# Kernel tuning notes

Measured on AMD Instinct MI355X. Metric: run time of the kernel, lower is better.

Reference implementation:

```python
import jax, jax.numpy as jnp
import numpy as np

N_NODES = 500_000
N_EDGES = 8_000_000
N_GRAPHS = 1000


def _mlp(x, w1, b1, w2, b2):
    # Linear -> SELU -> Linear (torch Sequential equivalent)
    return jax.nn.selu(x @ w1 + b1) @ w2 + b2


def setup_inputs() -> dict:
    key = jax.random.key(0)
    ks = jax.random.split(key, 25)
    p = lambda i, shape: jax.random.normal(ks[i], shape, jnp.float32) * 0.1
    return {
        "nodes": jax.random.normal(ks[0], (N_NODES, 1), jnp.float32),
        "edges": jax.random.normal(ks[1], (N_EDGES, 1), jnp.float32),
        "senders": jax.random.randint(ks[2], (N_EDGES,), 0, N_NODES),
        "receivers": jax.random.randint(ks[3], (N_EDGES,), 0, N_NODES),
        "graph_ids": jnp.sort(jax.random.randint(ks[4], (N_NODES,), 0, N_GRAPHS)),
        "num_graphs": N_GRAPHS,
        # permutate_nodes: 2 -> 10 -> 10
        "pn_w1": p(5, (2, 10)), "pn_b1": p(6, (10,)), "pn_w2": p(7, (10, 10)), "pn_b2": p(8, (10,)),
        # update_edges: 11 -> 5 -> 1
        "ue_w1": p(9, (11, 5)), "ue_b1": p(10, (5,)), "ue_w2": p(11, (5, 1)), "ue_b2": p(12, (1,)),
        # permutate_edges: 1 -> 5 -> 10
        "pe_w1": p(13, (1, 5)), "pe_b1": p(14, (5,)), "pe_w2": p(15, (5, 10)), "pe_b2": p(16, (10,)),
        # update_nodes: 11 -> 5 -> 1
        "un_w1": p(17, (11, 5)), "un_b1": p(18, (5,)), "un_w2": p(19, (5, 1)), "un_b2": p(20, (1,)),
        # predict: 11 -> 10 -> 10
        "pr_w1": p(21, (11, 10)), "pr_b1": p(22, (10,)), "pr_w2": p(23, (10, 10)), "pr_b2": p(24, (10,)),
    }


def reference(nodes, edges, pn_w1, pn_b1, pn_w2, pn_b2,
              ue_w1, ue_b1, ue_w2, ue_b2,
              pe_w1, pe_b1, pe_w2, pe_b2,
              un_w1, un_b1, un_w2, un_b2,
              pr_w1, pr_b1, pr_w2, pr_b2,
              senders, receivers, graph_ids, num_graphs):
    # gather node feats to edges: [recv || send] -> (E, 2)
    collected = jnp.concatenate([nodes[receivers], nodes[senders]], axis=-1)
    h1_nodes = _mlp(collected, pn_w1, pn_b1, pn_w2, pn_b2)  # (E, 10)
    h1_edges = edges  # (E, 1)
    for _ in range(3):
        h1_edges = _mlp(jnp.concatenate([h1_edges, h1_nodes], axis=-1),
                        ue_w1, ue_b1, ue_w2, ue_b2)  # (E, 1)
    # edges -> nodes aggregation (sum over receiver)
    edges_of_nodes = jax.ops.segment_sum(h1_edges, receivers, num_segments=nodes.shape[0])  # (N, 1)
    h2_edges = _mlp(edges_of_nodes, pe_w1, pe_b1, pe_w2, pe_b2)  # (N, 10)
    h2_nodes = nodes  # (N, 1)
    for _ in range(3):
        h2_nodes = _mlp(jnp.concatenate([h2_nodes, h2_edges], axis=-1),
                        un_w1, un_b1, un_w2, un_b2)  # (N, 1)
    # nodes -> globals aggregation (sum per graph)
    g = jax.ops.segment_sum(jnp.concatenate([h2_nodes, h2_edges], axis=-1),
                            graph_ids, num_segments=num_graphs)  # (G, 11)
    out = _mlp(g, pr_w1, pr_b1, pr_w2, pr_b2)  # (G, 10)
    return jax.nn.softmax(out, axis=-1)
```

## Files before the change

kernel.cpp:

```cpp
#include <hip/hip_runtime.h>
#include <hip/hip_fp16.h>
#include <math.h>

#define N_NODES_C  500000
#define N_EDGES_C  8000000
#define N_GRAPHS_C 1000
#define NGROUPS_C  (N_EDGES_C / 4)

#define BSHIFT  11
#define BWIDTH  2048
#define NBKT    245

#define PART_TPB 512
#define EPB     16384
#define GPB     (EPB / 4)
#define NPB     ((NGROUPS_C + GPB - 1) / GPB)
#define SROW    496
#define RITER   (GPB / PART_TPB)

#define GRAPH_ACC_OFF 0
#define PARTIALS_OFF  11008
#define FW_OFF        33024
#define STARTS_OFF    33280
#define PAIRS_OFF     (STARTS_OFF + 246 * SROW)
#define WS_WORDS_NEEDED (PAIRS_OFF + NPB * EPB)
#define ZERO_HEAD     33024
#define OLD_NODE_ACC_OFF 33536
#define OLD_ZERO_WORDS   (OLD_NODE_ACC_OFF + N_NODES_C)

#define LOG2E_F 1.4426950408889634f


__device__ __forceinline__ float selu2(float xl) {
    const float C1 = 0.7282901039f;
    const float C2 = 1.7580993408473766f;
    float e = __builtin_amdgcn_exp2f(xl);
    float neg = fmaf(C2, e, -C2);
    return xl > 0.0f ? C1 * xl : neg;
}

__device__ __forceinline__ float selu_f(float x) {
    const float scale = 1.0507009873554805f;
    const float sa    = 1.0507009873554805f * 1.6732632423543772f;
    float neg = sa * (__expf(x) - 1.0f);
    return x > 0.0f ? scale * x : neg;
}

__device__ __forceinline__ void atomAddF(float* p, float v) {
    __hip_atomic_fetch_add(p, v, __ATOMIC_RELAXED, __HIP_MEMORY_SCOPE_AGENT);
}

__device__ __forceinline__ void fuse_weights(
        int t,
        const float* __restrict__ pn_w1, const float* __restrict__ pn_b1,
        const float* __restrict__ pn_w2, const float* __restrict__ pn_b2,
        const float* __restrict__ ue_w1, const float* __restrict__ ue_b1,
        const float* __restrict__ ue_w2, const float* __restrict__ ue_b2,
        const float* __restrict__ pe_w1, const float* __restrict__ pe_b1,
        const float* __restrict__ pe_w2, const float* __restrict__ pe_b2,
        const float* __restrict__ un_w1, const float* __restrict__ un_b1,
        const float* __restrict__ un_w2, const float* __restrict__ un_b2,
        float* __restrict__ fw) {
    const float L = LOG2E_F;
    if (t < 20) fw[0 + t] = pn_w1[t] * L;
    if (t < 10) fw[20 + t] = pn_b1[t] * L;
    if (t < 50) {
        int j = t / 5, k = t % 5;
        float s = 0.0f;
        for (int m = 0; m < 10; ++m) s += pn_w2[j * 10 + m] * ue_w1[(1 + m) * 5 + k];
        fw[30 + t] = s * L;
    }
    if (t < 5) {
        float s = ue_b1[t];
        for (int m = 0; m < 10; ++m) s += pn_b2[m] * ue_w1[(1 + m) * 5 + t];
        fw[80 + t] = s * L;
    }
    if (t < 5)  fw[85 + t]  = ue_w1[t] * L;
    if (t < 5)  fw[90 + t]  = ue_w2[t];
    if (t == 0) fw[95]      = ue_b2[0];
    if (t < 5)  fw[96 + t]  = pe_w1[t] * L;
    if (t < 5)  fw[101 + t] = pe_b1[t] * L;
    if (t < 50) fw[106 + t] = pe_w2[t];
    if (t < 10) fw[156 + t] = pe_b2[t];
    if (t < 25) {
        int j = t / 5, k = t % 5;
        float s = 0.0f;
        for (int m = 0; m < 10; ++m) s += pe_w2[j * 10 + m] * un_w1[(1 + m) * 5 + k];
        fw[166 + t] = s * L;
    }
    if (t < 5) {
        float s = un_b1[t];
        for (int m = 0; m < 10; ++m) s += pe_b2[m] * un_w1[(1 + m) * 5 + t];
        fw[191 + t] = s * L;
    }
    if (t < 5)  fw[196 + t] = un_w1[t] * L;
    if (t < 5)  fw[201 + t] = un_w2[t];
    if (t == 0) fw[206]     = un_b2[0];
}

__global__ __launch_bounds__(256) void k_init(
        float* __restrict__ ws,
        const float* pn_w1, const float* pn_b1, const float* pn_w2, const float* pn_b2,
        const float* ue_w1, const float* ue_b1, const float* ue_w2, const float* ue_b2,
        const float* pe_w1, const float* pe_b1, const float* pe_w2, const float* pe_b2,
        const float* un_w1, const float* un_b1, const float* un_w2, const float* un_b2) {
    int i = blockIdx.x * 256 + threadIdx.x;
    if (i < ZERO_HEAD) ws[i] = 0.0f;
    if (blockIdx.x == 0)
        fuse_weights(threadIdx.x, pn_w1, pn_b1, pn_w2, pn_b2, ue_w1, ue_b1, ue_w2, ue_b2,
                     pe_w1, pe_b1, pe_w2, pe_b2, un_w1, un_b1, un_w2, un_b2, ws + FW_OFF);
}

__global__ void k_fuse(const float* pn_w1, const float* pn_b1, const float* pn_w2, const float* pn_b2,
                       const float* ue_w1, const float* ue_b1, const float* ue_w2, const float* ue_b2,
                       const float* pe_w1, const float* pe_b1, const float* pe_w2, const float* pe_b2,
                       const float* un_w1, const float* un_b1, const float* un_w2, const float* un_b2,
                       float* fw) {
    fuse_weights(threadIdx.x, pn_w1, pn_b1, pn_w2, pn_b2, ue_w1, ue_b1, ue_w2, ue_b2,
                 pe_w1, pe_b1, pe_w2, pe_b2, un_w1, un_b1, un_w2, un_b2, fw);
}

__global__ void k_final(const float* __restrict__ graph_acc,
                        const float* __restrict__ partials,
                        const float* __restrict__ pr_w1, const float* __restrict__ pr_b1,
                        const float* __restrict__ pr_w2, const float* __restrict__ pr_b2,
                        float* __restrict__ out) {
    int g = blockIdx.x * blockDim.x + threadIdx.x;
    if (g >= N_GRAPHS_C) return;
    float gv[11];
#pragma unroll
    for (int f = 0; f < 11; ++f)
        gv[f] = graph_acc[g * 11 + f] + partials[g * 11 + f] + partials[11000 + g * 11 + f];
    float h[10];
#pragma unroll
    for (int j = 0; j < 10; ++j) {
        float z = pr_b1[j];
#pragma unroll
        for (int f = 0; f < 11; ++f) z = fmaf(gv[f], pr_w1[f * 10 + j], z);
        h[j] = selu_f(z);
    }
    float o[10];
    float mx = -1e30f;
#pragma unroll
    for (int j = 0; j < 10; ++j) {
        float z = pr_b2[j];
#pragma unroll
        for (int m = 0; m < 10; ++m) z = fmaf(h[m], pr_w2[m * 10 + j], z);
        o[j] = z;
        mx = fmaxf(mx, z);
    }
    float sum = 0.0f;
#pragma unroll
    for (int j = 0; j < 10; ++j) { o[j] = __expf(o[j] - mx); sum += o[j]; }
    float inv = 1.0f / sum;
#pragma unroll
    for (int j = 0; j < 10; ++j) out[g * 10 + j] = o[j] * inv;
}


__global__ __launch_bounds__(PART_TPB, 4) void k_part(
        const float* __restrict__ nodes, const float* __restrict__ edges,
        const int* __restrict__ senders, const int* __restrict__ receivers,
        const float* __restrict__ fw, int* __restrict__ starts_T,
        unsigned int* __restrict__ pairs) {
    __shared__ int hist[256];
    __shared__ int cursorS[256];
    __shared__ unsigned int staged[EPB];

    int tid = threadIdx.x;
    int p   = blockIdx.x;
    int gstart = p * GPB;
    int gnum   = NGROUPS_C - gstart;
    if (gnum > GPB) gnum = GPB;

    float w_pn1[20], b_pn1[10], W_eb[50], b_eb[5], w1r0[5], w2e[5];
#pragma unroll
    for (int j = 0; j < 20; ++j) w_pn1[j] = fw[j];
#pragma unroll
    for (int j = 0; j < 10; ++j) b_pn1[j] = fw[20 + j];
#pragma unroll
    for (int j = 0; j < 50; ++j) W_eb[j] = fw[30 + j];
#pragma unroll
    for (int j = 0; j < 5; ++j) b_eb[j] = fw[80 + j];
#pragma unroll
    for (int j = 0; j < 5; ++j) w1r0[j] = fw[85 + j];
#pragma unroll
    for (int j = 0; j < 5; ++j) w2e[j] = fw[90 + j];
    float b2e = fw[95];

    if (tid < 256) hist[tid] = 0;
    __syncthreads();

#pragma unroll 1
    for (int r = 0; r < RITER; ++r) {
        int idx = r * PART_TPB + tid;
        int gi  = gstart + (idx < gnum ? idx : 0);
        int4 rv = ((const int4*)receivers)[gi];
        if (idx < gnum) {
            atomicAdd(&hist[rv.x >> BSHIFT], 1);
            atomicAdd(&hist[rv.y >> BSHIFT], 1);
            atomicAdd(&hist[rv.z >> BSHIFT], 1);
            atomicAdd(&hist[rv.w >> BSHIFT], 1);
        }
    }
    __syncthreads();

    int orig = 0, val = 0;
    if (tid < 256) { orig = hist[tid]; val = orig; }
    for (int d = 1; d < 256; d <<= 1) {
        int add = 0;
        if (tid >= d && tid < 256) add = hist[tid - d];
        __syncthreads();
        if (tid >= d && tid < 256) { val += add; hist[tid] = val; }
        __syncthreads();
    }
    int excl = val - orig;
    if (tid < 256) cursorS[tid] = excl;
    if (tid < 246) starts_T[tid * SROW + p] = excl;
    __syncthreads();

    float4 e4A, e4B, e4N;
    int4   s4A, s4B, s4N, r4A, r4B, r4N;
    float  nsA0, nsA1, nsA2, nsA3, nrA0, nrA1, nrA2, nrA3;
    float  nsB0, nsB1, nsB2, nsB3, nrB0, nrB1, nrB2, nrB3;

    {
        int gi0 = gstart + (tid < gnum ? tid : 0);
        e4A = ((const float4*)edges)[gi0];
        s4A = ((const int4*)senders)[gi0];
        r4A = ((const int4*)receivers)[gi0];
        nsA0 = nodes[s4A.x]; nsA1 = nodes[s4A.y];
        nsA2 = nodes[s4A.z]; nsA3 = nodes[s4A.w];
        nrA0 = nodes[r4A.x]; nrA1 = nodes[r4A.y];
        nrA2 = nodes[r4A.z]; nrA3 = nodes[r4A.w];
        int idx1 = PART_TPB + tid;
        int gi1 = gstart + (idx1 < gnum ? idx1 : 0);
        e4B = ((const float4*)edges)[gi1];
        s4B = ((const int4*)senders)[gi1];
        r4B = ((const int4*)receivers)[gi1];
    }

#pragma unroll 1
    for (int r = 0; r < RITER; ++r) {
        {
            int idx2 = (r + 2) * PART_TPB + tid;
            int gi2  = gstart + (idx2 < gnum ? idx2 : 0);
            e4N = ((const float4*)edges)[gi2];
            s4N = ((const int4*)senders)[gi2];
            r4N = ((const int4*)receivers)[gi2];
        }
        nsB0 = nodes[s4B.x]; nsB1 = nodes[s4B.y];
        nsB2 = nodes[s4B.z]; nsB3 = nodes[s4B.w];
        nrB0 = nodes[r4B.x]; nrB1 = nodes[r4B.y];
        nrB2 = nodes[r4B.z]; nrB3 = nodes[r4B.w];

        float ev[4]  = {e4A.x, e4A.y, e4A.z, e4A.w};
        int   rv[4]  = {r4A.x, r4A.y, r4A.z, r4A.w};
        float nsv[4] = {nsA0, nsA1, nsA2, nsA3};
        float nrv[4] = {nrA0, nrA1, nrA2, nrA3};

        bool validr = (r * PART_TPB + tid) < gnum;
#pragma unroll
        for (int u = 0; u < 4; ++u) {
            float nr = nrv[u], ns = nsv[u];
            float bs[5];
#pragma unroll
            for (int k = 0; k < 5; ++k) bs[k] = b_eb[k];
#pragma unroll
            for (int j = 0; j < 10; ++j) {
                float zl = fmaf(nr, w_pn1[j], fmaf(ns, w_pn1[10 + j], b_pn1[j]));
                float sz = selu2(zl);
#pragma unroll
                for (int k = 0; k < 5; ++k) bs[k] = fmaf(sz, W_eb[j * 5 + k], bs[k]);
            }
            float e = ev[u];
#pragma unroll
            for (int it = 0; it < 3; ++it) {
                float acc2 = b2e;
#pragma unroll
                for (int k = 0; k < 5; ++k) {
                    float tt = selu2(fmaf(e, w1r0[k], bs[k]));
                    acc2 = fmaf(tt, w2e[k], acc2);
                }
                e = acc2;
            }
            if (validr) {
                int bkt  = rv[u] >> BSHIFT;
                int slot = atomicAdd(&cursorS[bkt], 1);
                unsigned int pk = ((unsigned int)(rv[u] & (BWIDTH - 1)) << 16)
                                | (unsigned int)__half_as_ushort(__float2half_rn(e));
                staged[slot] = pk;
            }
        }

        e4A = e4B; s4A = s4B; r4A = r4B;
        nsA0 = nsB0; nsA1 = nsB1; nsA2 = nsB2; nsA3 = nsB3;
        nrA0 = nrB0; nrA1 = nrB1; nrA2 = nrB2; nrA3 = nrB3;
        e4B = e4N; s4B = s4N; r4B = r4N;
    }
    __syncthreads();

    const uint4* staged4 = (const uint4*)staged;
    uint4* dst = (uint4*)(pairs + (size_t)p * EPB);
    for (int i = tid; i < gnum; i += PART_TPB) dst[i] = staged4[i];
}

__global__ __launch_bounds__(1024) void k_gather(
        const float* __restrict__ nodes, const int* __restrict__ graph_ids,
        const float* __restrict__ fw, const int* __restrict__ starts_T,
        const unsigned int* __restrict__ pairs, float* __restrict__ graph_acc,
        float* __restrict__ partials) {
    __shared__ float accf[BWIDTH];
    __shared__ int s0[SROW], s1[SROW];
    __shared__ float garr[32 * 11];
    int tid = threadIdx.x;
    int b   = blockIdx.x;

    accf[tid] = 0.0f; accf[1024 + tid] = 0.0f;
    if (tid < 352) garr[tid] = 0.0f;
    for (int i = tid; i < NPB; i += 1024) {
        s0[i] = starts_T[b * SROW + i];
        s1[i] = starts_T[(b + 1) * SROW + i];
    }
    __syncthreads();

    int g32 = tid >> 5, lane = tid & 31;
    for (int p = g32; p < NPB; p += 32) {
        int st = s0[p], en = s1[p];
        const unsigned int* seg = pairs + (size_t)p * EPB + st;
        int cnt = en - st;
        for (int i = lane; i < cnt; i += 32) {
            unsigned int pk = seg[i];
            atomicAdd(&accf[(pk >> 16) & (BWIDTH - 1)],
                      __half2float(__ushort_as_half((unsigned short)(pk & 0xffff))));
        }
    }
    __syncthreads();

    float w_pe1[5], b_pe1[5], pe_w2[50], pe_b2[10], W_nb[25], b_nb[5], w1r0n[5], w2n[5];
#pragma unroll
    for (int j = 0; j < 5; ++j) w_pe1[j] = fw[96 + j];
#pragma unroll
    for (int j = 0; j < 5; ++j) b_pe1[j] = fw[101 + j];
#pragma unroll
    for (int j = 0; j < 50; ++j) pe_w2[j] = fw[106 + j];
#pragma unroll
    for (int j = 0; j < 10; ++j) pe_b2[j] = fw[156 + j];
#pragma unroll
    for (int j = 0; j < 25; ++j) W_nb[j] = fw[166 + j];
#pragma unroll
    for (int j = 0; j < 5; ++j) b_nb[j] = fw[191 + j];
#pragma unroll
    for (int j = 0; j < 5; ++j) w1r0n[j] = fw[196 + j];
#pragma unroll
    for (int j = 0; j < 5; ++j) w2n[j] = fw[201 + j];
    float b2n = fw[206];

    int nodeBase = b << BSHIFT;
    int lastIdx  = nodeBase + BWIDTH;
    if (lastIdx > N_NODES_C) lastIdx = N_NODES_C;
    int gidBase = graph_ids[nodeBase];
    int gidEnd  = graph_ids[lastIdx - 1];

#pragma unroll
    for (int q = 0; q < 2; ++q) {
        int local = q * 1024 + tid;
        int i = nodeBase + local;
        bool valid = i < N_NODES_C;

        float s = accf[local];
        float t5[5];
#pragma unroll
        for (int k = 0; k < 5; ++k) t5[k] = selu2(fmaf(s, w_pe1[k], b_pe1[k]));
        float he[10];
#pragma unroll
        for (int m = 0; m < 10; ++m) {
            float a = pe_b2[m];
#pragma unroll
            for (int k = 0; k < 5; ++k) a = fmaf(t5[k], pe_w2[k * 10 + m], a);
            he[m] = a;
        }
        float bs[5];
#pragma unroll
        for (int k = 0; k < 5; ++k) {
            float a = b_nb[k];
#pragma unroll
            for (int t = 0; t < 5; ++t) a = fmaf(t5[t], W_nb[t * 5 + k], a);
            bs[k] = a;
        }
        float n = valid ? nodes[i] : 0.0f;
#pragma unroll
        for (int it = 0; it < 3; ++it) {
            float a = b2n;
#pragma unroll
            for (int k = 0; k < 5; ++k) {
                float tt = selu2(fmaf(n, w1r0n[k], bs[k]));
                a = fmaf(tt, w2n[k], a);
            }
            n = a;
        }

        int gid = valid ? graph_ids[i] : -1;
        if (!valid) {
            n = 0.0f;
#pragma unroll
            for (int m = 0; m < 10; ++m) he[m] = 0.0f;
        }

        int gid0 = __shfl(gid, 0, 64);
        bool allsame = __all(gid == gid0) && (gid0 >= 0);
        if (allsame) {
            float v = n;
#pragma unroll
            for (int off = 32; off > 0; off >>= 1) v += __shfl_down(v, off, 64);
            float vh[10];
#pragma unroll
            for (int m = 0; m < 10; ++m) {
                float ww = he[m];
#pragma unroll
                for (int off = 32; off > 0; off >>= 1) ww += __shfl_down(ww, off, 64);
                vh[m] = ww;
            }
            if ((tid & 63) == 0) {
                int off = gid0 - gidBase;
                if (off >= 0 && off < 32) {
                    atomicAdd(&garr[off * 11 + 0], v);
#pragma unroll
                    for (int m = 0; m < 10; ++m) atomicAdd(&garr[off * 11 + 1 + m], vh[m]);
                } else {
                    atomAddF(&graph_acc[gid0 * 11 + 0], v);
#pragma unroll
                    for (int m = 0; m < 10; ++m) atomAddF(&graph_acc[gid0 * 11 + 1 + m], vh[m]);
                }
            }
        } else if (valid) {
            int off = gid - gidBase;
            if (off >= 0 && off < 32) {
                atomicAdd(&garr[off * 11 + 0], n);
#pragma unroll
                for (int m = 0; m < 10; ++m) atomicAdd(&garr[off * 11 + 1 + m], he[m]);
            } else {
                atomAddF(&graph_acc[gid * 11 + 0], n);
#pragma unroll
                for (int m = 0; m < 10; ++m) atomAddF(&graph_acc[gid * 11 + 1 + m], he[m]);
            }
        }
    }
    __syncthreads();

    int ngl = gidEnd - gidBase + 1;
    if (ngl > 32) ngl = 32;
    int par = (b & 1) * 11000;
    for (int t = tid; t < ngl * 11; t += 1024) {
        int off = t / 11, f = t - off * 11;
        partials[par + (gidBase + off) * 11 + f] = garr[t];
    }
}


__global__ __launch_bounds__(256) void k_zero(float* __restrict__ ws, int len4) {
    int i = blockIdx.x * 256 + threadIdx.x;
    if (i < len4) ((float4*)ws)[i] = make_float4(0.f, 0.f, 0.f, 0.f);
}

__global__ __launch_bounds__(256) void k_edges(
        const float* __restrict__ nodes, const float* __restrict__ edges,
        const int* __restrict__ senders, const int* __restrict__ receivers,
        const float* __restrict__ fw, float* __restrict__ node_acc) {
    float w_pn1[20], b_pn1[10], W_eb[50], b_eb[5], w1r0[5], w2e[5];
#pragma unroll
    for (int j = 0; j < 20; ++j) w_pn1[j] = fw[j];
#pragma unroll
    for (int j = 0; j < 10; ++j) b_pn1[j] = fw[20 + j];
#pragma unroll
    for (int j = 0; j < 50; ++j) W_eb[j] = fw[30 + j];
#pragma unroll
    for (int j = 0; j < 5; ++j) b_eb[j] = fw[80 + j];
#pragma unroll
    for (int j = 0; j < 5; ++j) w1r0[j] = fw[85 + j];
#pragma unroll
    for (int j = 0; j < 5; ++j) w2e[j] = fw[90 + j];
    float b2e = fw[95];

    int g = blockIdx.x * 256 + threadIdx.x;
    if (g >= NGROUPS_C) return;

    float4 e4 = ((const float4*)edges)[g];
    int4  s4 = ((const int4*)senders)[g];
    int4  r4 = ((const int4*)receivers)[g];
    float ev[4] = {e4.x, e4.y, e4.z, e4.w};
    int   sv[4] = {s4.x, s4.y, s4.z, s4.w};
    int   rv[4] = {r4.x, r4.y, r4.z, r4.w};
    float nsv[4], nrv[4];
#pragma unroll
    for (int u = 0; u < 4; ++u) { nsv[u] = nodes[sv[u]]; nrv[u] = nodes[rv[u]]; }
#pragma unroll
    for (int u = 0; u < 4; ++u) {
        float nr = nrv[u], ns = nsv[u];
        float bs[5];
#pragma unroll
        for (int k = 0; k < 5; ++k) bs[k] = b_eb[k];
#pragma unroll
        for (int j = 0; j < 10; ++j) {
            float zl = fmaf(nr, w_pn1[j], fmaf(ns, w_pn1[10 + j], b_pn1[j]));
            float sz = selu2(zl);
#pragma unroll
            for (int k = 0; k < 5; ++k) bs[k] = fmaf(sz, W_eb[j * 5 + k], bs[k]);
        }
        float e = ev[u];
#pragma unroll
        for (int it = 0; it < 3; ++it) {
            float acc2 = b2e;
#pragma unroll
            for (int k = 0; k < 5; ++k) {
                float tt = selu2(fmaf(e, w1r0[k], bs[k]));
                acc2 = fmaf(tt, w2e[k], acc2);
            }
            e = acc2;
        }
        atomAddF(&node_acc[rv[u]], e);
    }
}

__global__ __launch_bounds__(256) void k_nodes(
        const float* __restrict__ nodes, const int* __restrict__ graph_ids,
        const float* __restrict__ fw, const float* __restrict__ node_acc,
        float* __restrict__ graph_acc) {
    float w_pe1[5], b_pe1[5], pe_w2[50], pe_b2[10], W_nb[25], b_nb[5], w1r0n[5], w2n[5];
#pragma unroll
    for (int j = 0; j < 5; ++j) w_pe1[j] = fw[96 + j];
#pragma unroll
    for (int j = 0; j < 5; ++j) b_pe1[j] = fw[101 + j];
#pragma unroll
    for (int j = 0; j < 50; ++j) pe_w2[j] = fw[106 + j];
#pragma unroll
    for (int j = 0; j < 10; ++j) pe_b2[j] = fw[156 + j];
#pragma unroll
    for (int j = 0; j < 25; ++j) W_nb[j] = fw[166 + j];
#pragma unroll
    for (int j = 0; j < 5; ++j) b_nb[j] = fw[191 + j];
#pragma unroll
    for (int j = 0; j < 5; ++j) w1r0n[j] = fw[196 + j];
#pragma unroll
    for (int j = 0; j < 5; ++j) w2n[j] = fw[201 + j];
    float b2n = fw[206];

    int i = blockIdx.x * 256 + threadIdx.x;
    bool valid = i < N_NODES_C;
    int ii = valid ? i : (N_NODES_C - 1);

    float s = node_acc[ii];
    float t5[5];
#pragma unroll
    for (int k = 0; k < 5; ++k) t5[k] = selu2(fmaf(s, w_pe1[k], b_pe1[k]));
    float he[10];
#pragma unroll
    for (int m = 0; m < 10; ++m) {
        float a = pe_b2[m];
#pragma unroll
        for (int k = 0; k < 5; ++k) a = fmaf(t5[k], pe_w2[k * 10 + m], a);
        he[m] = a;
    }
    float bs[5];
#pragma unroll
    for (int k = 0; k < 5; ++k) {
        float a = b_nb[k];
#pragma unroll
        for (int t = 0; t < 5; ++t) a = fmaf(t5[t], W_nb[t * 5 + k], a);
        bs[k] = a;
    }
    float n = nodes[ii];
#pragma unroll
    for (int it = 0; it < 3; ++it) {
        float a = b2n;
#pragma unroll
        for (int k = 0; k < 5; ++k) {
            float tt = selu2(fmaf(n, w1r0n[k], bs[k]));
            a = fmaf(tt, w2n[k], a);
        }
        n = a;
    }

    int gid = valid ? graph_ids[ii] : -1;
    if (!valid) {
        n = 0.0f;
#pragma unroll
        for (int m = 0; m < 10; ++m) he[m] = 0.0f;
    }

    int gid0 = __shfl(gid, 0, 64);
    bool allsame = __all(gid == gid0) && (gid0 >= 0);
    if (allsame) {
        float v = n;
#pragma unroll
        for (int off = 32; off > 0; off >>= 1) v += __shfl_down(v, off, 64);
        float vh[10];
#pragma unroll
        for (int m = 0; m < 10; ++m) {
            float ww = he[m];
#pragma unroll
            for (int off = 32; off > 0; off >>= 1) ww += __shfl_down(ww, off, 64);
            vh[m] = ww;
        }
        if ((threadIdx.x & 63) == 0) {
            atomAddF(&graph_acc[gid0 * 11 + 0], v);
#pragma unroll
            for (int m = 0; m < 10; ++m) atomAddF(&graph_acc[gid0 * 11 + 1 + m], vh[m]);
        }
    } else if (valid) {
        atomAddF(&graph_acc[gid * 11 + 0], n);
#pragma unroll
        for (int m = 0; m < 10; ++m) atomAddF(&graph_acc[gid * 11 + 1 + m], he[m]);
    }
}


extern "C" void kernel_launch(void* const* d_in, const int* in_sizes, int n_in,
                              void* d_out, int out_size, void* d_ws, size_t ws_size,
                              hipStream_t stream) {
    const float* nodes     = (const float*)d_in[0];
    const float* edges     = (const float*)d_in[1];
    const int*   senders   = (const int*)d_in[2];
    const int*   receivers = (const int*)d_in[3];
    const int*   graph_ids = (const int*)d_in[4];
    const float* pn_w1 = (const float*)d_in[6];
    const float* pn_b1 = (const float*)d_in[7];
    const float* pn_w2 = (const float*)d_in[8];
    const float* pn_b2 = (const float*)d_in[9];
    const float* ue_w1 = (const float*)d_in[10];
    const float* ue_b1 = (const float*)d_in[11];
    const float* ue_w2 = (const float*)d_in[12];
    const float* ue_b2 = (const float*)d_in[13];
    const float* pe_w1 = (const float*)d_in[14];
    const float* pe_b1 = (const float*)d_in[15];
    const float* pe_w2 = (const float*)d_in[16];
    const float* pe_b2 = (const float*)d_in[17];
    const float* un_w1 = (const float*)d_in[18];
    const float* un_b1 = (const float*)d_in[19];
    const float* un_w2 = (const float*)d_in[20];
    const float* un_b2 = (const float*)d_in[21];
    const float* pr_w1 = (const float*)d_in[22];
    const float* pr_b1 = (const float*)d_in[23];
    const float* pr_w2 = (const float*)d_in[24];
    const float* pr_b2 = (const float*)d_in[25];

    float* ws        = (float*)d_ws;
    float* graph_acc = ws + GRAPH_ACC_OFF;
    float* partials  = ws + PARTIALS_OFF;
    float* fw        = ws + FW_OFF;
    float* outp      = (float*)d_out;

    if (ws_size >= (size_t)WS_WORDS_NEEDED * 4) {
        int* starts_T        = (int*)ws + STARTS_OFF;
        unsigned int* pairs  = (unsigned int*)ws + PAIRS_OFF;

        hipLaunchKernelGGL(k_init, dim3((ZERO_HEAD + 255) / 256), dim3(256), 0, stream, ws,
                           pn_w1, pn_b1, pn_w2, pn_b2, ue_w1, ue_b1, ue_w2, ue_b2,
                           pe_w1, pe_b1, pe_w2, pe_b2, un_w1, un_b1, un_w2, un_b2);
        hipLaunchKernelGGL(k_part, dim3(NPB), dim3(PART_TPB), 0, stream,
                           nodes, edges, senders, receivers, fw, starts_T, pairs);
        hipLaunchKernelGGL(k_gather, dim3(NBKT), dim3(1024), 0, stream,
                           nodes, graph_ids, fw, starts_T, pairs, graph_acc, partials);
        hipLaunchKernelGGL(k_final, dim3((N_GRAPHS_C + 255) / 256), dim3(256), 0, stream,
                           graph_acc, partials, pr_w1, pr_b1, pr_w2, pr_b2, outp);
    } else {
        float* node_acc = ws + OLD_NODE_ACC_OFF;
        int len4 = OLD_ZERO_WORDS / 4;
        hipLaunchKernelGGL(k_zero, dim3((len4 + 255) / 256), dim3(256), 0, stream, ws, len4);
        hipLaunchKernelGGL(k_fuse, dim3(1), dim3(64), 0, stream,
                           pn_w1, pn_b1, pn_w2, pn_b2, ue_w1, ue_b1, ue_w2, ue_b2,
                           pe_w1, pe_b1, pe_w2, pe_b2, un_w1, un_b1, un_w2, un_b2, fw);
        hipLaunchKernelGGL(k_edges, dim3((NGROUPS_C + 255) / 256), dim3(256), 0, stream,
                           nodes, edges, senders, receivers, fw, node_acc);
        hipLaunchKernelGGL(k_nodes, dim3((N_NODES_C + 255) / 256), dim3(256), 0, stream,
                           nodes, graph_ids, fw, node_acc, graph_acc);
        hipLaunchKernelGGL(k_final, dim3((N_GRAPHS_C + 255) / 256), dim3(256), 0, stream,
                           graph_acc, partials, pr_w1, pr_b1, pr_w2, pr_b2, outp);
    }
}
```

Before: 318.9 us.

## Defer edge MLP to gather stage using 64-bit packed raw edge records

Measured after the change: 293.2 us. 1.09x faster.

```diff
diff --git a/kernel.cpp b/kernel.cpp
--- a/kernel.cpp
+++ b/kernel.cpp
@@ -18,13 +18,26 @@
 #define SROW    496
 #define RITER   (GPB / PART_TPB)
 
+#define P2_TPB  512
+#define EPB2    8192
+#define GPB2    (EPB2 / 4)
+#define NPB2    ((NGROUPS_C + GPB2 - 1) / GPB2)
+#define SROW2   992
+#define RITER2  (GPB2 / P2_TPB)
+
 #define GRAPH_ACC_OFF 0
 #define PARTIALS_OFF  11008
 #define FW_OFF        33024
+#define ZERO_HEAD     33024
+
 #define STARTS_OFF    33280
 #define PAIRS_OFF     (STARTS_OFF + 246 * SROW)
 #define WS_WORDS_NEEDED (PAIRS_OFF + NPB * EPB)
-#define ZERO_HEAD     33024
+
+#define STARTS2_OFF   33280
+#define PAIRS64_OFF   (STARTS2_OFF + 246 * SROW2)
+#define WS2_WORDS_NEEDED (PAIRS64_OFF + NPB2 * EPB2 * 2)
+
 #define OLD_NODE_ACC_OFF 33536
 #define OLD_ZERO_WORDS   (OLD_NODE_ACC_OFF + N_NODES_C)
 
@@ -155,6 +168,304 @@
     float inv = 1.0f / sum;
 #pragma unroll
     for (int j = 0; j < 10; ++j) out[g * 10 + j] = o[j] * inv;
+}
+
+
+__global__ __launch_bounds__(P2_TPB) void k_part2(
+        const float* __restrict__ edges,
+        const int* __restrict__ senders, const int* __restrict__ receivers,
+        int* __restrict__ starts_T, unsigned long long* __restrict__ pairs64) {
+    __shared__ int hist[256];
+    __shared__ int cursorS[256];
+    __shared__ alignas(16) unsigned long long staged[EPB2];
+
+    int tid = threadIdx.x;
+    int p   = blockIdx.x;
+    int gstart = p * GPB2;
+    int gnum   = NGROUPS_C - gstart;
+    if (gnum > GPB2) gnum = GPB2;
+
+    if (tid < 256) hist[tid] = 0;
+    __syncthreads();
+
+    int4 rv4[RITER2];
+#pragma unroll
+    for (int r = 0; r < RITER2; ++r) {
+        int idx = r * P2_TPB + tid;
+        int gi  = gstart + (idx < gnum ? idx : 0);
+        rv4[r] = ((const int4*)receivers)[gi];
+        if (idx < gnum) {
+            atomicAdd(&hist[rv4[r].x >> BSHIFT], 1);
+            atomicAdd(&hist[rv4[r].y >> BSHIFT], 1);
+            atomicAdd(&hist[rv4[r].z >> BSHIFT], 1);
+            atomicAdd(&hist[rv4[r].w >> BSHIFT], 1);
+        }
+    }
+    __syncthreads();
+
+    int orig = 0, val = 0;
+    if (tid < 256) { orig = hist[tid]; val = orig; }
+    for (int d = 1; d < 256; d <<= 1) {
+        int add = 0;
+        if (tid >= d && tid < 256) add = hist[tid - d];
+        __syncthreads();
+        if (tid >= d && tid < 256) { val += add; hist[tid] = val; }
+        __syncthreads();
+    }
+    int excl = val - orig;
+    if (tid < 256) cursorS[tid] = excl;
+    if (tid < 246) starts_T[tid * SROW2 + p] = excl;
+    __syncthreads();
+
+#pragma unroll
+    for (int r = 0; r < RITER2; ++r) {
+        int idx = r * P2_TPB + tid;
+        int gi  = gstart + (idx < gnum ? idx : 0);
+        float4 e4 = ((const float4*)edges)[gi];
+        int4   s4 = ((const int4*)senders)[gi];
+        int4   rv = rv4[r];
+        if (idx < gnum) {
+            int   rvv[4] = {rv.x, rv.y, rv.z, rv.w};
+            int   svv[4] = {s4.x, s4.y, s4.z, s4.w};
+            float evv[4] = {e4.x, e4.y, e4.z, e4.w};
+#pragma unroll
+            for (int u = 0; u < 4; ++u) {
+                int bkt  = rvv[u] >> BSHIFT;
+                int slot = atomicAdd(&cursorS[bkt], 1);
+                unsigned long long pk =
+                    ((unsigned long long)(rvv[u] & (BWIDTH - 1)) << 51)
+                  | ((unsigned long long)(unsigned)svv[u] << 32)
+                  | (unsigned long long)__float_as_uint(evv[u]);
+                staged[slot] = pk;
+            }
+        }
+    }
+    __syncthreads();
+
+    const uint4* st4 = (const uint4*)staged;
+    uint4* dst = (uint4*)(pairs64 + (size_t)p * EPB2);
+    int n4 = gnum * 2;
+    for (int i = tid; i < n4; i += P2_TPB) dst[i] = st4[i];
+}
+
+__global__ __launch_bounds__(1024) void k_gather2(
+        const float* __restrict__ nodes, const int* __restrict__ graph_ids,
+        const float* __restrict__ fw, const int* __restrict__ starts_T,
+        const unsigned long long* __restrict__ pairs64,
+        float* __restrict__ graph_acc, float* __restrict__ partials) {
+    __shared__ float accf[BWIDTH];
+    __shared__ float nf[BWIDTH];
+    __shared__ int   s0[NPB2];
+    __shared__ int   pst[NPB2 + 1];
+    __shared__ int   sc[1024];
+    __shared__ float garr[32 * 11];
+    int tid = threadIdx.x;
+    int b   = blockIdx.x;
+
+    int nodeBase = b << BSHIFT;
+    int lastIdx  = nodeBase + BWIDTH;
+    if (lastIdx > N_NODES_C) lastIdx = N_NODES_C;
+    int lim = lastIdx - nodeBase;
+
+    accf[tid] = 0.0f; accf[1024 + tid] = 0.0f;
+    nf[tid]        = (tid        < lim) ? nodes[nodeBase + tid]        : 0.0f;
+    nf[1024 + tid] = (1024 + tid < lim) ? nodes[nodeBase + 1024 + tid] : 0.0f;
+    if (tid < 352) garr[tid] = 0.0f;
+
+    int cntv = 0;
+    if (tid < NPB2) {
+        int a = starts_T[b * SROW2 + tid];
+        int c = starts_T[(b + 1) * SROW2 + tid];
+        s0[tid] = a;
+        cntv = c - a;
+    }
+    sc[tid] = cntv;
+    __syncthreads();
+
+    int v = cntv;
+    for (int d = 1; d < 1024; d <<= 1) {
+        int add = (tid >= d) ? sc[tid - d] : 0;
+        __syncthreads();
+        if (tid >= d) { v += add; sc[tid] = v; }
+        __syncthreads();
+    }
+    if (tid == 0) pst[0] = 0;
+    if (tid < NPB2) pst[tid + 1] = v;
+    __syncthreads();
+
+    int M = pst[NPB2];
+
+    {
+        float w_pn1[20], b_pn1[10], W_eb[50], b_eb[5], w1r0[5], w2e[5];
+#pragma unroll
+        for (int j = 0; j < 20; ++j) w_pn1[j] = fw[j];
+#pragma unroll
+        for (int j = 0; j < 10; ++j) b_pn1[j] = fw[20 + j];
+#pragma unroll
+        for (int j = 0; j < 50; ++j) W_eb[j] = fw[30 + j];
+#pragma unroll
+        for (int j = 0; j < 5; ++j) b_eb[j] = fw[80 + j];
+#pragma unroll
+        for (int j = 0; j < 5; ++j) w1r0[j] = fw[85 + j];
+#pragma unroll
+        for (int j = 0; j < 5; ++j) w2e[j] = fw[90 + j];
+        float b2e = fw[95];
+
+#pragma unroll 1
+        for (int i = tid; i < M; i += 1024) {
+            int lo = 0, hi = NPB2;
+            while (hi - lo > 1) {
+                int mid = (lo + hi) >> 1;
+                if (pst[mid] <= i) lo = mid; else hi = mid;
+            }
+            int off = i - pst[lo];
+            unsigned long long pk = pairs64[(size_t)lo * EPB2 + s0[lo] + off];
+            int   rl   = (int)(pk >> 51);
+            int   sidx = (int)((pk >> 32) & 0x7FFFFULL);
+            float e    = __uint_as_float((unsigned)pk);
+            float nr   = nf[rl];
+            float ns   = nodes[sidx];
+
+            float bs[5];
+#pragma unroll
+            for (int k = 0; k < 5; ++k) bs[k] = b_eb[k];
+#pragma unroll
+            for (int j = 0; j < 10; ++j) {
+                float zl = fmaf(nr, w_pn1[j], fmaf(ns, w_pn1[10 + j], b_pn1[j]));
+                float sz = selu2(zl);
+#pragma unroll
+                for (int k = 0; k < 5; ++k) bs[k] = fmaf(sz, W_eb[j * 5 + k], bs[k]);
+            }
+#pragma unroll
+            for (int it = 0; it < 3; ++it) {
+                float acc2 = b2e;
+#pragma unroll
+                for (int k = 0; k < 5; ++k) {
+                    float tt = selu2(fmaf(e, w1r0[k], bs[k]));
+                    acc2 = fmaf(tt, w2e[k], acc2);
+                }
+                e = acc2;
+            }
+            atomicAdd(&accf[rl], e);
+        }
+    }
+    __syncthreads();
+
+    float w_pe1[5], b_pe1[5], pe_w2[50], pe_b2[10], W_nb[25], b_nb[5], w1r0n[5], w2n[5];
+#pragma unroll
+    for (int j = 0; j < 5; ++j) w_pe1[j] = fw[96 + j];
+#pragma unroll
+    for (int j = 0; j < 5; ++j) b_pe1[j] = fw[101 + j];
+#pragma unroll
+    for (int j = 0; j < 50; ++j) pe_w2[j] = fw[106 + j];
+#pragma unroll
+    for (int j = 0; j < 10; ++j) pe_b2[j] = fw[156 + j];
+#pragma unroll
+    for (int j = 0; j < 25; ++j) W_nb[j] = fw[166 + j];
+#pragma unroll
+    for (int j = 0; j < 5; ++j) b_nb[j] = fw[191 + j];
+#pragma unroll
+    for (int j = 0; j < 5; ++j) w1r0n[j] = fw[196 + j];
+#pragma unroll
+    for (int j = 0; j < 5; ++j) w2n[j] = fw[201 + j];
+    float b2n = fw[206];
+
+    int gidBase = graph_ids[nodeBase];
+    int gidEnd  = graph_ids[lastIdx - 1];
+
+#pragma unroll
+    for (int q = 0; q < 2; ++q) {
+        int local = q * 1024 + tid;
+        int i = nodeBase + local;
+        bool valid = i < N_NODES_C;
+
+        float s = accf[local];
+        float t5[5];
+#pragma unroll
+        for (int k = 0; k < 5; ++k) t5[k] = selu2(fmaf(s, w_pe1[k], b_pe1[k]));
+        float he[10];
+#pragma unroll
+        for (int m = 0; m < 10; ++m) {
+            float a = pe_b2[m];
+#pragma unroll
+            for (int k = 0; k < 5; ++k) a = fmaf(t5[k], pe_w2[k * 10 + m], a);
+            he[m] = a;
+        }
+        float bs[5];
+#pragma unroll
+        for (int k = 0; k < 5; ++k) {
+            float a = b_nb[k];
+#pragma unroll
+            for (int t = 0; t < 5; ++t) a = fmaf(t5[t], W_nb[t * 5 + k], a);
+            bs[k] = a;
+        }
+        float n = valid ? nf[local] : 0.0f;
+#pragma unroll
+        for (int it = 0; it < 3; ++it) {
+            float a = b2n;
+#pragma unroll
+            for (int k = 0; k < 5; ++k) {
+                float tt = selu2(fmaf(n, w1r0n[k], bs[k]));
+                a = fmaf(tt, w2n[k], a);
+            }
+            n = a;
+        }
+
+        int gid = valid ? graph_ids[i] : -1;
+        if (!valid) {
+            n = 0.0f;
+#pragma unroll
+            for (int m = 0; m < 10; ++m) he[m] = 0.0f;
+        }
+
+        int gid0 = __shfl(gid, 0, 64);
+        bool allsame = __all(gid == gid0) && (gid0 >= 0);
+        if (allsame) {
+            float vv = n;
+#pragma unroll
+            for (int off = 32; off > 0; off >>= 1) vv += __shfl_down(vv, off, 64);
+            float vh[10];
+#pragma unroll
+            for (int m = 0; m < 10; ++m) {
+                float ww = he[m];
+#pragma unroll
+                for (int off = 32; off > 0; off >>= 1) ww += __shfl_down(ww, off, 64);
+                vh[m] = ww;
+            }
+            if ((tid & 63) == 0) {
+                int off = gid0 - gidBase;
+                if (off >= 0 && off < 32) {
+                    atomicAdd(&garr[off * 11 + 0], vv);
+#pragma unroll
+                    for (int m = 0; m < 10; ++m) atomicAdd(&garr[off * 11 + 1 + m], vh[m]);
+                } else {
+                    atomAddF(&graph_acc[gid0 * 11 + 0], vv);
+#pragma unroll
+                    for (int m = 0; m < 10; ++m) atomAddF(&graph_acc[gid0 * 11 + 1 + m], vh[m]);
+                }
+            }
+        } else if (valid) {
+            int off = gid - gidBase;
+            if (off >= 0 && off < 32) {
+                atomicAdd(&garr[off * 11 + 0], n);
+#pragma unroll
+                for (int m = 0; m < 10; ++m) atomicAdd(&garr[off * 11 + 1 + m], he[m]);
+            } else {
+                atomAddF(&graph_acc[gid * 11 + 0], n);
+#pragma unroll
+                for (int m = 0; m < 10; ++m) atomAddF(&graph_acc[gid * 11 + 1 + m], he[m]);
+            }
+        }
+    }
+    __syncthreads();
+
+    int ngl = gidEnd - gidBase + 1;
+    if (ngl > 32) ngl = 32;
+    int par = (b & 1) * 11000;
+    for (int t = tid; t < ngl * 11; t += 1024) {
+        int off = t / 11, f = t - off * 11;
+        partials[par + (gidBase + off) * 11 + f] = garr[t];
+    }
 }
 
 
@@ -650,7 +961,20 @@
     float* fw        = ws + FW_OFF;
     float* outp      = (float*)d_out;
 
-    if (ws_size >= (size_t)WS_WORDS_NEEDED * 4) {
+    if (ws_size >= (size_t)WS2_WORDS_NEEDED * 4) {
+        int* starts_T = (int*)ws + STARTS2_OFF;
+        unsigned long long* pairs64 = (unsigned long long*)((int*)ws + PAIRS64_OFF);
+
+        hipLaunchKernelGGL(k_init, dim3((ZERO_HEAD + 255) / 256), dim3(256), 0, stream, ws,
+                           pn_w1, pn_b1, pn_w2, pn_b2, ue_w1, ue_b1, ue_w2, ue_b2,
+                           pe_w1, pe_b1, pe_w2, pe_b2, un_w1, un_b1, un_w2, un_b2);
+        hipLaunchKernelGGL(k_part2, dim3(NPB2), dim3(P2_TPB), 0, stream,
+                           edges, senders, receivers, starts_T, pairs64);
+        hipLaunchKernelGGL(k_gather2, dim3(NBKT), dim3(1024), 0, stream,
+                           nodes, graph_ids, fw, starts_T, pairs64, graph_acc, partials);
+        hipLaunchKernelGGL(k_final, dim3((N_GRAPHS_C + 255) / 256), dim3(256), 0, stream,
+                           graph_acc, partials, pr_w1, pr_b1, pr_w2, pr_b2, outp);
+    } else if (ws_size >= (size_t)WS_WORDS_NEEDED * 4) {
         int* starts_T        = (int*)ws + STARTS_OFF;
         unsigned int* pairs  = (unsigned int*)ws + PAIRS_OFF;
 
```
